# Optimization experiments

Measured on AMD Instinct MI355X. Metric: run time of the kernel, lower is better.

## Reference

```python
import jax, jax.numpy as jnp
import numpy as np

EMBED_DIM = 1024
NUM_HEADS = 16
HEAD_DIM = EMBED_DIM // NUM_HEADS
B, T = 4, 2048


def setup_inputs() -> dict:
    key = jax.random.key(0)
    ks = jax.random.split(key, 5)
    s = 0.02
    return {
        "x": jax.random.normal(ks[0], (B, T, EMBED_DIM), dtype=jnp.float32),
        "W_qkv": jax.random.normal(ks[1], (EMBED_DIM, 3 * EMBED_DIM), dtype=jnp.float32) * s,
        "b_qkv": jnp.zeros((3 * EMBED_DIM,), dtype=jnp.float32),
        "W_proj": jax.random.normal(ks[2], (EMBED_DIM, EMBED_DIM), dtype=jnp.float32) * s,
        "b_proj": jnp.zeros((EMBED_DIM,), dtype=jnp.float32),
    }


def reference(x, W_qkv, b_qkv, W_proj, b_proj):
    # Dropout disabled (eval mode) for deterministic reference.
    Bsz, Tlen, C = x.shape
    qkv = x @ W_qkv + b_qkv                          # [B,T,3C]
    q, k, v = jnp.split(qkv, 3, axis=-1)
    def heads(t):  # [B,T,C] -> [B,H,T,Dh]
        return t.reshape(Bsz, Tlen, NUM_HEADS, HEAD_DIM).transpose(0, 2, 1, 3)
    q, k, v = heads(q), heads(k), heads(v)
    scale = HEAD_DIM ** -0.5
    wei = jnp.einsum("bhqd,bhkd->bhqk", q, k) * scale  # [B,H,T,T]
    causal = jnp.tril(jnp.ones((Tlen, Tlen), dtype=bool))
    wei = jnp.where(causal[None, None], wei, -jnp.inf)
    wei = jax.nn.softmax(wei, axis=-1)
    out = jnp.einsum("bhqk,bhkd->bhqd", wei, v)        # [B,H,T,Dh]
    out = out.transpose(0, 2, 1, 3).reshape(Bsz, Tlen, C)
    return out @ W_proj + b_proj
```

## Files before the change

kernel.cpp:

```cpp
#include <hip/hip_runtime.h>

#define DEV __device__ __forceinline__

using u16 = unsigned short;
using u32 = unsigned int;
typedef __attribute__((ext_vector_type(8)))  short  short8;
typedef __attribute__((ext_vector_type(8)))  u16    ushort8;
typedef __attribute__((ext_vector_type(4)))  u16    us4;
typedef __attribute__((ext_vector_type(4)))  float  f32x4;
typedef __attribute__((ext_vector_type(16))) float  f32x16;

constexpr int BB = 4;
constexpr int TT = 2048;
constexpr int CC = 1024;
constexpr int HH = 16;
constexpr int DD = 64;
constexpr int MM = BB * TT;
constexpr int N1 = 3 * CC;

DEV u16 f2bf(float f) {
    unsigned u = __float_as_uint(f);
    unsigned r = (u + 0x7FFFu + ((u >> 16) & 1u)) >> 16;
    return (u16)r;
}

DEV u32 cvtpk(float lo, float hi) {
    u32 r;
    asm("v_cvt_pk_bf16_f32 %0, %1, %2" : "=v"(r) : "v"(lo), "v"(hi));
    return r;
}

DEV void gload_lds16(const void* g, void* l) {
    __builtin_amdgcn_global_load_lds((const __attribute__((address_space(1))) void*)g,
                                     (__attribute__((address_space(3))) void*)l,
                                     16, 0, 0);
}

__global__ void k_cvt_x(const float* __restrict__ src, u16* __restrict__ dst) {
    int i = (blockIdx.x * 256 + threadIdx.x) * 8;
    f32x4 a = *(const f32x4*)(src + i);
    f32x4 b = *(const f32x4*)(src + i + 4);
    ushort8 u;
    u[0] = f2bf(a[0]); u[1] = f2bf(a[1]); u[2] = f2bf(a[2]); u[3] = f2bf(a[3]);
    u[4] = f2bf(b[0]); u[5] = f2bf(b[1]); u[6] = f2bf(b[2]); u[7] = f2bf(b[3]);
    *(ushort8*)(dst + i) = u;
}

__global__ __launch_bounds__(256) void k_transpose_cvt2(const float* __restrict__ src,
                                                        u16* __restrict__ dst,
                                                        int Kd, int Nd) {
    __shared__ u16 tile[64][66];
    const int t = threadIdx.x;
    const int k0 = blockIdx.y * 64, n0 = blockIdx.x * 64;
    const int c = t & 63, r0 = (t >> 6) * 16;
#pragma unroll
    for (int i = 0; i < 16; ++i)
        tile[r0 + i][c] = f2bf(src[(size_t)(k0 + r0 + i) * Nd + n0 + c]);
    __syncthreads();
    const int kc = (t & 7) * 8, nn = t >> 3;
#pragma unroll
    for (int h = 0; h < 2; ++h) {
        int n = nn + h * 32;
        ushort8 v;
#pragma unroll
        for (int j = 0; j < 8; ++j) v[j] = tile[kc + j][n];
        *(ushort8*)(dst + (size_t)(n0 + n) * Kd + k0 + kc) = v;
    }
}

DEV void stage_tile(const u16* __restrict__ Ag, const u16* __restrict__ Bg, int kt,
                    u16* As, u16* Bs, int lane, int wid) {
#pragma unroll
    for (int p = 0; p < 2; ++p) {
        int cb = p * 256 + wid * 64;
        int chunk = cb + lane;
        int row = chunk >> 2, kc = chunk & 3;
        gload_lds16(Ag + (size_t)row * 1024 + kt + kc * 8, As + cb * 8);
        gload_lds16(Bg + (size_t)row * 1024 + kt + kc * 8, Bs + cb * 8);
    }
}

DEV void gemm_mainloop3(const u16* __restrict__ Ag, const u16* __restrict__ Bg,
                        u16 (*As)[4096], u16 (*Bs)[4096], f32x4 acc[4][4]) {
    const int tid = threadIdx.x, lane = tid & 63, wid = tid >> 6;
    const int wr = wid >> 1, wc = wid & 1;
    stage_tile(Ag, Bg, 0,  As[0], Bs[0], lane, wid);
    stage_tile(Ag, Bg, 32, As[1], Bs[1], lane, wid);
    int cur = 0;
#pragma unroll 1
    for (int t = 0; t < 32; ++t) {
        if (t == 31) asm volatile("s_waitcnt vmcnt(0)" ::: "memory");
        else         asm volatile("s_waitcnt vmcnt(4)" ::: "memory");
        __builtin_amdgcn_s_barrier();
        if (t + 2 < 32) {
            int nb = cur + 2; if (nb > 2) nb -= 3;
            stage_tile(Ag, Bg, (t + 2) * 32, As[nb], Bs[nb], lane, wid);
        }
        short8 aF[4], bF[4];
#pragma unroll
        for (int m = 0; m < 4; ++m)
            aF[m] = *(const short8*)&As[cur][(wr * 64 + m * 16 + (lane & 15)) * 32 + (lane >> 4) * 8];
#pragma unroll
        for (int n = 0; n < 4; ++n)
            bF[n] = *(const short8*)&Bs[cur][(wc * 64 + n * 16 + (lane & 15)) * 32 + (lane >> 4) * 8];
        __builtin_amdgcn_s_setprio(1);
#pragma unroll
        for (int m = 0; m < 4; ++m)
#pragma unroll
            for (int n = 0; n < 4; ++n)
                acc[m][n] = __builtin_amdgcn_mfma_f32_16x16x32_bf16(aF[m], bF[n], acc[m][n], 0, 0, 0);
        __builtin_amdgcn_s_setprio(0);
        cur = (cur == 2) ? 0 : cur + 1;
    }
}

__global__ __launch_bounds__(256) void k_gemm_qkv(const u16* __restrict__ xb,
                                                  const u16* __restrict__ wt,
                                                  const float* __restrict__ bqkv,
                                                  u16* __restrict__ qb,
                                                  u16* __restrict__ kb,
                                                  u16* __restrict__ vtb) {
    __shared__ u16 As[3][4096], Bs[3][4096];
    f32x4 acc[4][4];
#pragma unroll
    for (int m = 0; m < 4; ++m)
#pragma unroll
        for (int n = 0; n < 4; ++n) acc[m][n] = (f32x4){0.f, 0.f, 0.f, 0.f};
    const int rowBase = blockIdx.x * 128, colBase = blockIdx.y * 128;
    gemm_mainloop3(xb + (size_t)rowBase * 1024, wt + (size_t)colBase * 1024, As, Bs, acc);
    const int lane = threadIdx.x & 63, wid = threadIdx.x >> 6;
    const int wr = wid >> 1, wc = wid & 1;
#pragma unroll
    for (int n = 0; n < 4; ++n) {
        int gn = colBase + wc * 64 + n * 16 + (lane & 15);
        float bias = bqkv[gn];
        int which = gn >> 10, cc = gn & 1023, hh = cc >> 6, d = cc & 63;
        if (which == 2) {
            u16* vdst = vtb + ((size_t)hh * DD + d) * TT;
#pragma unroll
            for (int m = 0; m < 4; ++m) {
                int gm = rowBase + wr * 64 + m * 16 + (lane >> 4) * 4;
                int b = gm >> 11, t = gm & 2047;
                us4 pv;
#pragma unroll
                for (int r = 0; r < 4; ++r) pv[r] = f2bf(acc[m][n][r] + bias);
                *(us4*)(vdst + (size_t)b * (HH * DD * TT) + t) = pv;
            }
        } else {
            u16* dst = (which == 0 ? qb : kb);
            float sc = (which == 0) ? 0.125f : 1.0f;
#pragma unroll
            for (int m = 0; m < 4; ++m) {
#pragma unroll
                for (int r = 0; r < 4; ++r) {
                    int gm = rowBase + wr * 64 + m * 16 + (lane >> 4) * 4 + r;
                    int b = gm >> 11, t = gm & 2047;
                    dst[(((size_t)b * HH + hh) * TT + t) * DD + d] = f2bf((acc[m][n][r] + bias) * sc);
                }
            }
        }
    }
}

__global__ __launch_bounds__(256) void k_gemm_proj(const u16* __restrict__ ob,
                                                   const u16* __restrict__ wt,
                                                   const float* __restrict__ bproj,
                                                   float* __restrict__ out) {
    __shared__ u16 As[3][4096], Bs[3][4096];
    f32x4 acc[4][4];
#pragma unroll
    for (int m = 0; m < 4; ++m)
#pragma unroll
        for (int n = 0; n < 4; ++n) acc[m][n] = (f32x4){0.f, 0.f, 0.f, 0.f};
    const int rowBase = blockIdx.x * 128, colBase = blockIdx.y * 128;
    gemm_mainloop3(ob + (size_t)rowBase * 1024, wt + (size_t)colBase * 1024, As, Bs, acc);
    const int lane = threadIdx.x & 63, wid = threadIdx.x >> 6;
    const int wr = wid >> 1, wc = wid & 1;
#pragma unroll
    for (int n = 0; n < 4; ++n) {
        int gn = colBase + wc * 64 + n * 16 + (lane & 15);
        float bias = bproj[gn];
#pragma unroll
        for (int m = 0; m < 4; ++m) {
#pragma unroll
            for (int r = 0; r < 4; ++r) {
                int gm = rowBase + wr * 64 + m * 16 + (lane >> 4) * 4 + r;
                out[(size_t)gm * 1024 + gn] = acc[m][n][r] + bias;
            }
        }
    }
}

DEV void attn_stage(const u16* __restrict__ kb_hb, const u16* __restrict__ vtb_hb,
                    int j, u16* Kd, u16* Vd, int tid) {
    int row = tid >> 3, sw = (tid & 7) ^ (row & 7);
    int cb8 = (tid & ~63) * 8;
    gload_lds16(kb_hb + (size_t)(j * 64 + row) * DD + sw * 8, Kd + cb8);
    gload_lds16(vtb_hb + (size_t)row * TT + j * 64 + sw * 8,  Vd + cb8);
}

__global__ __launch_bounds__(512) void k_attn2(const u16* __restrict__ qb,
                                               const u16* __restrict__ kb,
                                               const u16* __restrict__ vtb,
                                               u16* __restrict__ ob) {
    __shared__ u16 Kt[3][4096];
    __shared__ u16 Vs[3][4096];

    const int tid = threadIdx.x, lane = tid & 63, w = tid >> 6;
    const int h = lane >> 5, l31 = lane & 31;
    const int bh = blockIdx.x;
    const int qi = 7 - blockIdx.y;
    const size_t hb = (size_t)bh * (TT * DD);
    const int qw = qi * 256 + w * 32;
    const int nt_blk = 4 * qi + 4;
    const int nt_w = (qw >> 6) + 1;
    const u16* kb_hb = kb + hb;
    const u16* vtb_hb = vtb + hb;

    short8 qf[4];
#pragma unroll
    for (int df = 0; df < 4; ++df)
        qf[df] = *(const short8*)(qb + hb + (size_t)(qw + l31) * DD + df * 16 + h * 8);

    f32x16 o0, o1;
#pragma unroll
    for (int r = 0; r < 16; ++r) { o0[r] = 0.f; o1[r] = 0.f; }
    float mrun = -1e30f, lrun = 0.f;

    attn_stage(kb_hb, vtb_hb, 0, Kt[0], Vs[0], tid);
    attn_stage(kb_hb, vtb_hb, 1, Kt[1], Vs[1], tid);

    int cur = 0;
    for (int j = 0; j < nt_blk; ++j) {
        if (j == nt_blk - 1) asm volatile("s_waitcnt vmcnt(0)" ::: "memory");
        else                 asm volatile("s_waitcnt vmcnt(2)" ::: "memory");
        __builtin_amdgcn_s_barrier();
        if (j + 2 < nt_blk) {
            int nb = cur + 2; if (nb > 2) nb -= 3;
            attn_stage(kb_hb, vtb_hb, j + 2, Kt[nb], Vs[nb], tid);
        }
        if (j < nt_w) {
            f32x16 s0, s1;
#pragma unroll
            for (int r = 0; r < 16; ++r) { s0[r] = 0.f; s1[r] = 0.f; }
            __builtin_amdgcn_s_setprio(1);
#pragma unroll
            for (int df = 0; df < 4; ++df) {
                int colsw = df * 2 + h;
                int sw = (colsw ^ (l31 & 7)) * 8;
                short8 k0 = *(const short8*)&Kt[cur][l31 * 64 + sw];
                short8 k1 = *(const short8*)&Kt[cur][(l31 + 32) * 64 + sw];
                s0 = __builtin_amdgcn_mfma_f32_32x32x16_bf16(k0, qf[df], s0, 0, 0, 0);
                s1 = __builtin_amdgcn_mfma_f32_32x32x16_bf16(k1, qf[df], s1, 0, 0, 0);
            }
            __builtin_amdgcn_s_setprio(0);

            if (j == nt_w - 1) {
                int qrel = qw + l31 - j * 64;
#pragma unroll
                for (int r = 0; r < 16; ++r) {
                    int kk = (r & 3) + 8 * (r >> 2) + 4 * h;
                    if (kk      > qrel) s0[r] = -1e30f;
                    if (kk + 32 > qrel) s1[r] = -1e30f;
                }
            }

            float pm = -1e30f;
#pragma unroll
            for (int r = 0; r < 16; ++r) pm = fmaxf(pm, fmaxf(s0[r], s1[r]));
            pm = fmaxf(pm, __shfl_xor(pm, 32));
            if (!__all(pm <= mrun + 8.f)) {
                float mnew = fmaxf(mrun, pm);
                float sc = __expf(mrun - mnew);
                mrun = mnew;
                lrun *= sc;
#pragma unroll
                for (int r = 0; r < 16; ++r) {
                    float scr = __shfl(sc, (r & 3) + 8 * (r >> 2) + 4 * h);
                    o0[r] *= scr; o1[r] *= scr;
                }
            }
            float sum = 0.f;
#pragma unroll
            for (int r = 0; r < 16; ++r) {
                float p0 = __expf(s0[r] - mrun); s0[r] = p0; sum += p0;
                float p1 = __expf(s1[r] - mrun); s1[r] = p1; sum += p1;
            }
            sum += __shfl_xor(sum, 32);
            lrun += sum;

            __builtin_amdgcn_s_setprio(1);
#pragma unroll
            for (int f = 0; f < 4; ++f) {
                const f32x16& P = (f >= 2) ? s1 : s0;
                u32 A0, A1, B0, B1;
                if (f & 1) { A0 = cvtpk(P[8],  P[9]);  A1 = cvtpk(P[10], P[11]);
                             B0 = cvtpk(P[12], P[13]); B1 = cvtpk(P[14], P[15]); }
                else       { A0 = cvtpk(P[0],  P[1]);  A1 = cvtpk(P[2],  P[3]);
                             B0 = cvtpk(P[4],  P[5]);  B1 = cvtpk(P[6],  P[7]);  }
                u32 U0 = h ? B0 : A0, U1 = h ? B1 : A1;
                u32 V0 = h ? A0 : B0, V1 = h ? A1 : B1;
                u32 W0 = (u32)__shfl_xor((int)V0, 32);
                u32 W1 = (u32)__shfl_xor((int)V1, 32);
                union { u32 u[4]; short8 s; } pa;
                pa.u[0] = h ? W0 : U0; pa.u[1] = h ? W1 : U1;
                pa.u[2] = h ? U0 : W0; pa.u[3] = h ? U1 : W1;
#pragma unroll
                for (int dt = 0; dt < 2; ++dt) {
                    int row = dt * 32 + l31;
                    short8 vf = *(const short8*)&Vs[cur][row * 64 + (((f * 2 + h) ^ (row & 7)) * 8)];
                    if (dt == 0) o0 = __builtin_amdgcn_mfma_f32_32x32x16_bf16(pa.s, vf, o0, 0, 0, 0);
                    else         o1 = __builtin_amdgcn_mfma_f32_32x32x16_bf16(pa.s, vf, o1, 0, 0, 0);
                }
            }
            __builtin_amdgcn_s_setprio(0);
        }
        cur = (cur == 2) ? 0 : cur + 1;
    }

    const int b = bh >> 4, head = bh & 15;
    float linv = 1.f / lrun;
#pragma unroll
    for (int r = 0; r < 16; ++r) {
        float li = __shfl(linv, (r & 3) + 8 * (r >> 2) + 4 * h);
        int q = qw + (r & 3) + 8 * (r >> 2) + 4 * h;
        size_t rb = ((size_t)(b * TT + q)) * CC + head * 64;
        ob[rb + l31]      = f2bf(o0[r] * li);
        ob[rb + 32 + l31] = f2bf(o1[r] * li);
    }
}

extern "C" void kernel_launch(void* const* d_in, const int* in_sizes, int n_in,
                              void* d_out, int out_size, void* d_ws, size_t ws_size,
                              hipStream_t stream) {
    const float* x     = (const float*)d_in[0];
    const float* Wqkv  = (const float*)d_in[1];
    const float* bqkv  = (const float*)d_in[2];
    const float* Wproj = (const float*)d_in[3];
    const float* bproj = (const float*)d_in[4];
    float* out = (float*)d_out;

    char* ws = (char*)d_ws;
    u16* xb    = (u16*)(ws + 0);
    u16* wqkvT = (u16*)(ws + 16777216);
    u16* wprojT= (u16*)(ws + 23068672);
    u16* qb    = (u16*)(ws + 25165824);
    u16* kb    = (u16*)(ws + 41943040);
    u16* vtb   = (u16*)(ws + 58720256);
    u16* ob    = xb;

    k_cvt_x<<<dim3(MM * CC / (256 * 8)), 256, 0, stream>>>(x, xb);
    k_transpose_cvt2<<<dim3(N1 / 64, CC / 64), 256, 0, stream>>>(Wqkv, wqkvT, CC, N1);
    k_transpose_cvt2<<<dim3(CC / 64, CC / 64), 256, 0, stream>>>(Wproj, wprojT, CC, CC);
    k_gemm_qkv<<<dim3(MM / 128, N1 / 128), 256, 0, stream>>>(xb, wqkvT, bqkv, qb, kb, vtb);
    k_attn2<<<dim3(BB * HH, TT / 256), 512, 0, stream>>>(qb, kb, vtb, ob);
    k_gemm_proj<<<dim3(MM / 128, CC / 128), 256, 0, stream>>>(ob, wprojT, bproj, out);
}
```

Before: 270.4 us.

## Use BK=64 double-buffered GEMM mainloop with XOR-swizzled LDS layout

Replaces the triple-buffered BK=32 GEMM mainloop with a double-buffered BK=64 loop in both the QKV and projection GEMMs, halving the number of barriers and iterations. Global-to-LDS loads now place 16-byte chunks at XOR-swizzled positions so the fragment reads avoid LDS bank conflicts. The trade-off is less prefetch depth: each iteration waits on vmcnt(0) for the next tile, and LDS use grows from 48KB to 64KB per block, which may lower occupancy.

```diff
diff --git a/kernel.cpp b/kernel.cpp
--- a/kernel.cpp
+++ b/kernel.cpp
@@ -68,49 +68,57 @@
     }
 }
 
-DEV void stage_tile(const u16* __restrict__ Ag, const u16* __restrict__ Bg, int kt,
-                    u16* As, u16* Bs, int lane, int wid) {
-#pragma unroll
-    for (int p = 0; p < 2; ++p) {
+DEV void stage_tile64(const u16* __restrict__ Ag, const u16* __restrict__ Bg, int kt,
+                      u16* As, u16* Bs, int lane, int wid) {
+#pragma unroll
+    for (int p = 0; p < 4; ++p) {
         int cb = p * 256 + wid * 64;
-        int chunk = cb + lane;
-        int row = chunk >> 2, kc = chunk & 3;
-        gload_lds16(Ag + (size_t)row * 1024 + kt + kc * 8, As + cb * 8);
-        gload_lds16(Bg + (size_t)row * 1024 + kt + kc * 8, Bs + cb * 8);
-    }
-}
-
-DEV void gemm_mainloop3(const u16* __restrict__ Ag, const u16* __restrict__ Bg,
-                        u16 (*As)[4096], u16 (*Bs)[4096], f32x4 acc[4][4]) {
+        int c = cb + lane;
+        int row = c >> 3, slot = c & 7;
+        int g = slot ^ (row & 7);
+        gload_lds16(Ag + (size_t)row * 1024 + kt + g * 8, As + cb * 8);
+        gload_lds16(Bg + (size_t)row * 1024 + kt + g * 8, Bs + cb * 8);
+    }
+}
+
+DEV void gemm_ml4(const u16* __restrict__ Ag, const u16* __restrict__ Bg,
+                  u16 (*As)[8192], u16 (*Bs)[8192], f32x4 acc[4][4]) {
     const int tid = threadIdx.x, lane = tid & 63, wid = tid >> 6;
     const int wr = wid >> 1, wc = wid & 1;
-    stage_tile(Ag, Bg, 0,  As[0], Bs[0], lane, wid);
-    stage_tile(Ag, Bg, 32, As[1], Bs[1], lane, wid);
+    stage_tile64(Ag, Bg, 0, As[0], Bs[0], lane, wid);
+    asm volatile("s_waitcnt vmcnt(0)" ::: "memory");
     int cur = 0;
 #pragma unroll 1
-    for (int t = 0; t < 32; ++t) {
-        if (t == 31) asm volatile("s_waitcnt vmcnt(0)" ::: "memory");
-        else         asm volatile("s_waitcnt vmcnt(4)" ::: "memory");
+    for (int t = 0; t < 16; ++t) {
         __builtin_amdgcn_s_barrier();
-        if (t + 2 < 32) {
-            int nb = cur + 2; if (nb > 2) nb -= 3;
-            stage_tile(Ag, Bg, (t + 2) * 32, As[nb], Bs[nb], lane, wid);
-        }
-        short8 aF[4], bF[4];
-#pragma unroll
-        for (int m = 0; m < 4; ++m)
-            aF[m] = *(const short8*)&As[cur][(wr * 64 + m * 16 + (lane & 15)) * 32 + (lane >> 4) * 8];
-#pragma unroll
-        for (int n = 0; n < 4; ++n)
-            bF[n] = *(const short8*)&Bs[cur][(wc * 64 + n * 16 + (lane & 15)) * 32 + (lane >> 4) * 8];
-        __builtin_amdgcn_s_setprio(1);
-#pragma unroll
-        for (int m = 0; m < 4; ++m)
-#pragma unroll
-            for (int n = 0; n < 4; ++n)
-                acc[m][n] = __builtin_amdgcn_mfma_f32_16x16x32_bf16(aF[m], bF[n], acc[m][n], 0, 0, 0);
-        __builtin_amdgcn_s_setprio(0);
-        cur = (cur == 2) ? 0 : cur + 1;
+        __builtin_amdgcn_sched_barrier(0);
+        if (t + 1 < 16)
+            stage_tile64(Ag, Bg, (t + 1) * 64, As[cur ^ 1], Bs[cur ^ 1], lane, wid);
+#pragma unroll
+        for (int kh = 0; kh < 2; ++kh) {
+            const int g = kh * 4 + (lane >> 4);
+            short8 aF[4], bF[4];
+#pragma unroll
+            for (int m = 0; m < 4; ++m) {
+                int row = wr * 64 + m * 16 + (lane & 15);
+                aF[m] = *(const short8*)&As[cur][row * 64 + ((g ^ (row & 7)) * 8)];
+            }
+#pragma unroll
+            for (int n = 0; n < 4; ++n) {
+                int row = wc * 64 + n * 16 + (lane & 15);
+                bF[n] = *(const short8*)&Bs[cur][row * 64 + ((g ^ (row & 7)) * 8)];
+            }
+            __builtin_amdgcn_s_setprio(1);
+#pragma unroll
+            for (int m = 0; m < 4; ++m)
+#pragma unroll
+                for (int n = 0; n < 4; ++n)
+                    acc[m][n] = __builtin_amdgcn_mfma_f32_16x16x32_bf16(aF[m], bF[n], acc[m][n], 0, 0, 0);
+            __builtin_amdgcn_s_setprio(0);
+        }
+        asm volatile("s_waitcnt vmcnt(0)" ::: "memory");
+        __builtin_amdgcn_sched_barrier(0);
+        cur ^= 1;
     }
 }
 
@@ -120,14 +128,14 @@
                                                   u16* __restrict__ qb,
                                                   u16* __restrict__ kb,
                                                   u16* __restrict__ vtb) {
-    __shared__ u16 As[3][4096], Bs[3][4096];
+    __shared__ u16 As[2][8192], Bs[2][8192];
     f32x4 acc[4][4];
 #pragma unroll
     for (int m = 0; m < 4; ++m)
 #pragma unroll
         for (int n = 0; n < 4; ++n) acc[m][n] = (f32x4){0.f, 0.f, 0.f, 0.f};
     const int rowBase = blockIdx.x * 128, colBase = blockIdx.y * 128;
-    gemm_mainloop3(xb + (size_t)rowBase * 1024, wt + (size_t)colBase * 1024, As, Bs, acc);
+    gemm_ml4(xb + (size_t)rowBase * 1024, wt + (size_t)colBase * 1024, As, Bs, acc);
     const int lane = threadIdx.x & 63, wid = threadIdx.x >> 6;
     const int wr = wid >> 1, wc = wid & 1;
 #pragma unroll
@@ -166,14 +174,14 @@
                                                    const u16* __restrict__ wt,
                                                    const float* __restrict__ bproj,
                                                    float* __restrict__ out) {
-    __shared__ u16 As[3][4096], Bs[3][4096];
+    __shared__ u16 As[2][8192], Bs[2][8192];
     f32x4 acc[4][4];
 #pragma unroll
     for (int m = 0; m < 4; ++m)
 #pragma unroll
         for (int n = 0; n < 4; ++n) acc[m][n] = (f32x4){0.f, 0.f, 0.f, 0.f};
     const int rowBase = blockIdx.x * 128, colBase = blockIdx.y * 128;
-    gemm_mainloop3(ob + (size_t)rowBase * 1024, wt + (size_t)colBase * 1024, As, Bs, acc);
+    gemm_ml4(ob + (size_t)rowBase * 1024, wt + (size_t)colBase * 1024, As, Bs, acc);
     const int lane = threadIdx.x & 63, wid = threadIdx.x >> 6;
     const int wr = wid >> 1, wc = wid & 1;
 #pragma unroll
```

After: 251.6 us. -6.9%, faster.
